# Kernel optimization log

Measured on AMD Instinct MI355X. Metric: run time of the kernel, lower is better.

## Reference

```python
import jax, jax.numpy as jnp
import numpy as np

N_NODES = 20000
N_EDGES = 640000
NUM_COUNTS = 64
NUM_FEATS = 128


def setup_inputs() -> dict:
    key = jax.random.key(0)
    k1, k2, k3, k4, k5 = jax.random.split(key, 5)
    cnt = jax.random.uniform(k1, (N_EDGES, NUM_COUNTS), dtype=jnp.float32)
    embedding = jax.random.normal(k2, (N_NODES, NUM_FEATS), dtype=jnp.float32)
    importance = jax.random.normal(k3, (NUM_COUNTS, NUM_FEATS), dtype=jnp.float32)
    src = jax.random.randint(k4, (N_EDGES,), 0, N_NODES, dtype=jnp.int32)
    # ensure every node has >=1 incoming edge so the normalization divide is well-defined
    dst = jax.random.permutation(k5, jnp.arange(N_EDGES, dtype=jnp.int32) % N_NODES)
    return {"cnt": cnt, "embedding": embedding, "importance": importance, "src": src, "dst": dst}


def reference(cnt, embedding, importance, src, dst):
    # weight = softmax over the num_counts axis (dim=0)
    weight = jax.nn.softmax(importance, axis=0)            # [C, F]
    edge_score = cnt @ weight                               # [E, F] dense GEMM
    msgs = embedding[src] * edge_score                      # [E, F] u_mul_e
    new_embedding = jax.ops.segment_sum(msgs, dst, num_segments=N_NODES)      # [N, F]
    node_score = jax.ops.segment_sum(edge_score, dst, num_segments=N_NODES)   # [N, F]
    return new_embedding / node_score
```

## Files before the change

### kernel.cpp

```cpp
#include <hip/hip_runtime.h>
#include <hip/hip_bf16.h>
#include <stdint.h>

#define NN 20000
#define NE 640000
#define NC 64
#define NF 128
#define CAP 32
#define NPW 5
#define WPB 4
#define NSTEP (2 * NPW)

typedef __attribute__((ext_vector_type(8))) short short8;
typedef __attribute__((ext_vector_type(8))) __bf16 bf16x8;
typedef __attribute__((ext_vector_type(2))) __bf16 bf16x2;
typedef __attribute__((ext_vector_type(4))) float floatx4;
typedef __attribute__((ext_vector_type(4))) unsigned int uintx4;

static __device__ __forceinline__ unsigned short f2bf(float f) {
  union { float f; unsigned int i; } v; v.f = f;
  unsigned int x = v.i;
  x += 0x7fffu + ((x >> 16) & 1u);
  return (unsigned short)(x >> 16);
}

static __device__ __forceinline__ unsigned int pk2(float a, float b) {
#if __has_builtin(__builtin_amdgcn_cvt_pk_bf16_f32)
  bf16x2 r = __builtin_amdgcn_cvt_pk_bf16_f32(a, b);
  return __builtin_bit_cast(unsigned int, r);
#else
  return (unsigned int)f2bf(a) | ((unsigned int)f2bf(b) << 16);
#endif
}

static __device__ __forceinline__ short8 cvt8(floatx4 lo, floatx4 hi) {
  uintx4 u;
  u.x = pk2(lo[0], lo[1]); u.y = pk2(lo[2], lo[3]);
  u.z = pk2(hi[0], hi[1]); u.w = pk2(hi[2], hi[3]);
  return __builtin_bit_cast(short8, u);
}

static __device__ __forceinline__ float frcp(float x) {
#if __has_builtin(__builtin_amdgcn_rcpf)
  return __builtin_amdgcn_rcpf(x);
#else
  return 1.0f / x;
#endif
}

#define GLOAD_LDS(gp, lp)                                                      \
  __builtin_amdgcn_global_load_lds(                                           \
      (const __attribute__((address_space(1))) void*)(gp),                     \
      (__attribute__((address_space(3))) void*)(lp), 16, 0, 0)

__global__ __launch_bounds__(256) void pre_kernel(
    const float* __restrict__ imp, unsigned short* __restrict__ wpack,
    int* __restrict__ counts, int ncounts) {
  __shared__ float w_s[NC][NF];
  const int tid = threadIdx.x;
  for (int i = blockIdx.x * 256 + tid; i < ncounts; i += gridDim.x * 256)
    counts[i] = 0;

  if (blockIdx.x != 0) return;
  if (tid < NF) {
    float v[NC];
    float mx = -1e30f;
#pragma unroll
    for (int c = 0; c < NC; ++c) { v[c] = imp[c * NF + tid]; mx = fmaxf(mx, v[c]); }
    float s = 0.f;
#pragma unroll
    for (int c = 0; c < NC; ++c) { v[c] = __expf(v[c] - mx); s += v[c]; }
    float inv = 1.0f / s;
#pragma unroll
    for (int c = 0; c < NC; ++c) w_s[c][tid] = v[c] * inv;
  }
  __syncthreads();
#pragma unroll
  for (int idx = 0; idx < NC * NF; idx += 256) {
    int i2 = idx + tid;
    int j  = i2 & 7;
    int l  = (i2 >> 3) & 63;
    int ks = (i2 >> 9) & 1;
    int nt = i2 >> 10;
    int k  = ks * 32 + (l >> 4) * 8 + j;
    int f  = 8 * (l & 15) + nt;
    wpack[i2] = f2bf(w_s[k][f]);
  }
}

__global__ __launch_bounds__(256) void bin_kernel(
    const int* __restrict__ dst, int* __restrict__ counts,
    int* __restrict__ elist, int cstride) {
  int e = blockIdx.x * 256 + threadIdx.x;
  if (e < NE) {
    int n = dst[e];
    int slot = atomicAdd(&counts[(size_t)n * cstride], 1);
    if (slot < CAP) elist[n * CAP + slot] = e;
  }
}

__global__ __launch_bounds__(256) void node_kernel(
    const float* __restrict__ cnt,
    const float* __restrict__ emb,
    const int* __restrict__ srcp,
    const int* __restrict__ elist,
    const unsigned short* __restrict__ wpack,
    float* __restrict__ out)
{
  __shared__ float cnt_s[WPB][2][16 * NC];

  const int tid = threadIdx.x;
  const int wid = tid >> 6;
  const int lane = tid & 63;
  const int m = lane & 15;
  const int q = lane >> 4;
  const int base = (blockIdx.x * WPB + wid) * NPW;

  short8 wf[8][2];
#pragma unroll
  for (int nt = 0; nt < 8; ++nt)
#pragma unroll
    for (int ks = 0; ks < 2; ++ks)
      wf[nt][ks] = *(const short8*)(wpack + ((nt * 2 + ks) * 64 + lane) * 8);

  int e_cur = elist[(size_t)base * CAP + (lane & 31)];
  int s_cur = srcp[e_cur];
  int pe = 0, ps = 0;

#pragma unroll
  for (int j = 0; j < 4; ++j) {
    int rl = 4 * j + q;
    int eid = __shfl(e_cur, rl);
    int cs = m ^ (rl & 7);
    GLOAD_LDS(cnt + (size_t)eid * NC + cs * 4, &cnt_s[wid][0][j * 256]);
  }

  float ea[8], sa[8];

#pragma unroll
  for (int s = 0; s < NSTEP; ++s) {
    const int h = s & 1;
    const int node = base + (s >> 1);
    const int cbuf = s & 1;
    const bool more = (s + 1 < NSTEP);

    if (h == 0) {
#pragma unroll
      for (int t = 0; t < 8; ++t) { ea[t] = 0.f; sa[t] = 0.f; }
      if (s + 2 < NSTEP) pe = elist[(size_t)(node + 1) * CAP + (lane & 31)];
    } else if (more) {
      ps = srcp[pe];
    }

    if (more) {
#pragma unroll
      for (int j = 0; j < 4; ++j) {
        int rl = 4 * j + q;
        int eid = __shfl(h ? pe : e_cur, (h ? 0 : 16) + rl);
        int cs = m ^ (rl & 7);
        GLOAD_LDS(cnt + (size_t)eid * NC + cs * 4,
                  &cnt_s[wid][cbuf ^ 1][j * 256]);
      }
      asm volatile("s_waitcnt vmcnt(4)" ::: "memory");
    } else {
      asm volatile("s_waitcnt vmcnt(0)" ::: "memory");
    }

    const float* cb = cnt_s[wid][cbuf];
    const int sw = m & 7;
    const int rb = m * NC;
    floatx4 c0 = *(const floatx4*)&cb[rb + ((2 * q)     ^ sw) * 4];
    floatx4 c1 = *(const floatx4*)&cb[rb + ((2 * q + 1) ^ sw) * 4];
    floatx4 c2 = *(const floatx4*)&cb[rb + ((8 + 2 * q) ^ sw) * 4];
    floatx4 c3 = *(const floatx4*)&cb[rb + ((9 + 2 * q) ^ sw) * 4];
    short8 a0 = cvt8(c0, c1);
    short8 a1 = cvt8(c2, c3);

    floatx4 acc[8];
#pragma unroll
    for (int nt = 0; nt < 8; ++nt) {
#pragma unroll
      for (int r = 0; r < 4; ++r) acc[nt][r] = 0.f;
      acc[nt] = __builtin_amdgcn_mfma_f32_16x16x32_bf16(
          __builtin_bit_cast(bf16x8, a0), __builtin_bit_cast(bf16x8, wf[nt][0]),
          acc[nt], 0, 0, 0);
      acc[nt] = __builtin_amdgcn_mfma_f32_16x16x32_bf16(
          __builtin_bit_cast(bf16x8, a1), __builtin_bit_cast(bf16x8, wf[nt][1]),
          acc[nt], 0, 0, 0);
    }

#pragma unroll
    for (int nt = 0; nt < 8; ++nt)
#pragma unroll
      for (int r = 0; r < 4; ++r) sa[nt] += acc[nt][r];

#pragma unroll
    for (int r = 0; r < 4; ++r) {
      int sv = __shfl(s_cur, h * 16 + 4 * q + r);
      const float* er = emb + (size_t)sv * NF + m * 8;
      floatx4 ev0 = *(const floatx4*)er;
      floatx4 ev1 = *(const floatx4*)(er + 4);
#pragma unroll
      for (int nt = 0; nt < 4; ++nt)
        ea[nt] = fmaf(acc[nt][r], ev0[nt], ea[nt]);
#pragma unroll
      for (int nt = 4; nt < 8; ++nt)
        ea[nt] = fmaf(acc[nt][r], ev1[nt - 4], ea[nt]);
    }

    if (h == 1) {
#pragma unroll
      for (int t = 0; t < 8; ++t) {
        ea[t] += __shfl_xor(ea[t], 16, 64);
        ea[t] += __shfl_xor(ea[t], 32, 64);
        sa[t] += __shfl_xor(sa[t], 16, 64);
        sa[t] += __shfl_xor(sa[t], 32, 64);
      }
      if (lane < 16) {
        floatx4 o0, o1;
#pragma unroll
        for (int p = 0; p < 4; ++p) {
          o0[p] = ea[p] * frcp(sa[p]);
          o1[p] = ea[p + 4] * frcp(sa[p + 4]);
        }
        float* op = out + (size_t)node * NF + m * 8;
        *(floatx4*)op = o0;
        *(floatx4*)(op + 4) = o1;
      }
      if (more) { e_cur = pe; s_cur = ps; }
    }
  }
}

extern "C" void kernel_launch(void* const* d_in, const int* in_sizes, int n_in,
                              void* d_out, int out_size, void* d_ws, size_t ws_size,
                              hipStream_t stream) {
  const float* cnt = (const float*)d_in[0];
  const float* emb = (const float*)d_in[1];
  const float* imp = (const float*)d_in[2];
  const int* src = (const int*)d_in[3];
  const int* dst = (const int*)d_in[4];
  float* out = (float*)d_out;

  char* ws = (char*)d_ws;
  unsigned short* wpack = (unsigned short*)(ws);

  const size_t need_padded = 16384 + (size_t)NN * 32 + (size_t)NN * CAP * 4;
  int cstride;
  int* counts;
  int* elist;
  if (ws_size >= need_padded) {
    cstride = 8;
    counts = (int*)(ws + 16384);
    elist  = (int*)(ws + 16384 + (size_t)NN * 32);
  } else {
    cstride = 1;
    counts = (int*)(ws + 16384);
    elist  = (int*)(ws + 98304);
  }

  const int ncounts = NN * cstride;
  pre_kernel<<<(ncounts + 255) / 256, 256, 0, stream>>>(imp, wpack, counts, ncounts);
  bin_kernel<<<(NE + 255) / 256, 256, 0, stream>>>(dst, counts, elist, cstride);
  node_kernel<<<NN / (WPB * NPW), 256, 0, stream>>>(cnt, emb, src, elist, wpack, out);
}
```

Measured before the change: 309.8 us.

## Pre-convert cnt to bf16 during binning and stage weights in LDS

Binning is fused with a pass that converts the whole fp32 cnt matrix to a bf16 copy in workspace. The node kernel then gathers half-width rows into LDS and reads the packed softmax weights from shared memory instead of holding them in registers. This is meant to cut gather bytes and register pressure in the node kernel. In exchange it adds a full extra read of cnt plus a bf16 write, so total memory traffic goes up. The new path needs a large workspace and falls back to the old fp32 kernel when that is unavailable.

After: 347.3 us. 12.1% more time.

```diff
diff --git a/kernel.cpp b/kernel.cpp
--- a/kernel.cpp
+++ b/kernel.cpp
@@ -88,6 +88,28 @@
   }
 }
 
+__global__ __launch_bounds__(256) void bin_conv_kernel(
+    const float* __restrict__ cnt, const int* __restrict__ dst,
+    int* __restrict__ counts, int* __restrict__ elist,
+    unsigned short* __restrict__ cntbf) {
+  int e = blockIdx.x * 256 + threadIdx.x;
+  if (e >= NE) return;
+  int n = dst[e];
+  int slot = atomicAdd(&counts[(size_t)n * 8], 1);
+  if (slot < CAP) elist[n * CAP + slot] = e;
+
+  const floatx4* s4 = (const floatx4*)(cnt + (size_t)e * NC);
+  uintx4* d4 = (uintx4*)(cntbf + (size_t)e * NC);
+#pragma unroll
+  for (int k = 0; k < 8; ++k) {
+    floatx4 f0 = s4[2 * k], f1 = s4[2 * k + 1];
+    uintx4 u;
+    u.x = pk2(f0[0], f0[1]); u.y = pk2(f0[2], f0[3]);
+    u.z = pk2(f1[0], f1[1]); u.w = pk2(f1[2], f1[3]);
+    d4[k] = u;
+  }
+}
+
 __global__ __launch_bounds__(256) void bin_kernel(
     const int* __restrict__ dst, int* __restrict__ counts,
     int* __restrict__ elist, int cstride) {
@@ -100,14 +122,15 @@
 }
 
 __global__ __launch_bounds__(256) void node_kernel(
-    const float* __restrict__ cnt,
+    const unsigned short* __restrict__ cntbf,
     const float* __restrict__ emb,
     const int* __restrict__ srcp,
     const int* __restrict__ elist,
     const unsigned short* __restrict__ wpack,
     float* __restrict__ out)
 {
-  __shared__ float cnt_s[WPB][2][16 * NC];
+  __shared__ short cnt_s[WPB][2][16 * NC];
+  __shared__ short wpack_s[NC * NF];
 
   const int tid = threadIdx.x;
   const int wid = tid >> 6;
@@ -116,6 +139,133 @@
   const int q = lane >> 4;
   const int base = (blockIdx.x * WPB + wid) * NPW;
 
+#pragma unroll
+  for (int k = 0; k < 4; ++k) {
+    int idx = (tid * 4 + k) * 8;
+    *(short8*)&wpack_s[idx] = *(const short8*)&wpack[idx];
+  }
+  __syncthreads();
+
+  int e_cur = elist[(size_t)base * CAP + (lane & 31)];
+  int s_cur = srcp[e_cur];
+  int pe = 0, ps = 0;
+
+  const int rr = lane >> 3;
+  const int pp = lane & 7;
+
+#pragma unroll
+  for (int j = 0; j < 2; ++j) {
+    int row = j * 8 + rr;
+    int eid = __shfl(e_cur, row);
+    int c = pp ^ (row & 7);
+    GLOAD_LDS(cntbf + (size_t)eid * NC + c * 8, &cnt_s[wid][0][j * 512]);
+  }
+
+  float ea[8], sa[8];
+
+#pragma unroll
+  for (int s = 0; s < NSTEP; ++s) {
+    const int h = s & 1;
+    const int node = base + (s >> 1);
+    const int cbuf = s & 1;
+    const bool more = (s + 1 < NSTEP);
+
+    if (h == 0) {
+#pragma unroll
+      for (int t = 0; t < 8; ++t) { ea[t] = 0.f; sa[t] = 0.f; }
+      if (s + 2 < NSTEP) pe = elist[(size_t)(node + 1) * CAP + (lane & 31)];
+    } else if (more) {
+      ps = srcp[pe];
+    }
+
+    if (more) {
+#pragma unroll
+      for (int j = 0; j < 2; ++j) {
+        int row = j * 8 + rr;
+        int eid = __shfl(h ? pe : e_cur, (h ? 0 : 16) + row);
+        int c = pp ^ (row & 7);
+        GLOAD_LDS(cntbf + (size_t)eid * NC + c * 8,
+                  &cnt_s[wid][cbuf ^ 1][j * 512]);
+      }
+      asm volatile("s_waitcnt vmcnt(2)" ::: "memory");
+    } else {
+      asm volatile("s_waitcnt vmcnt(0)" ::: "memory");
+    }
+
+    const short* cb = cnt_s[wid][cbuf];
+    short8 a0 = *(const short8*)&cb[m * NC + ((q       ^ (m & 7)) * 8)];
+    short8 a1 = *(const short8*)&cb[m * NC + (((4 + q) ^ (m & 7)) * 8)];
+
+    floatx4 acc[8];
+#pragma unroll
+    for (int nt = 0; nt < 8; ++nt) {
+#pragma unroll
+      for (int r = 0; r < 4; ++r) acc[nt][r] = 0.f;
+      short8 w0 = *(const short8*)&wpack_s[((nt * 2 + 0) * 64 + lane) * 8];
+      short8 w1 = *(const short8*)&wpack_s[((nt * 2 + 1) * 64 + lane) * 8];
+      acc[nt] = __builtin_amdgcn_mfma_f32_16x16x32_bf16(
+          __builtin_bit_cast(bf16x8, a0), __builtin_bit_cast(bf16x8, w0),
+          acc[nt], 0, 0, 0);
+      acc[nt] = __builtin_amdgcn_mfma_f32_16x16x32_bf16(
+          __builtin_bit_cast(bf16x8, a1), __builtin_bit_cast(bf16x8, w1),
+          acc[nt], 0, 0, 0);
+    }
+
+#pragma unroll
+    for (int nt = 0; nt < 8; ++nt)
+#pragma unroll
+      for (int r = 0; r < 4; ++r) sa[nt] += acc[nt][r];
+
+#pragma unroll
+    for (int r = 0; r < 4; ++r) {
+      int sv = __shfl(s_cur, h * 16 + 4 * q + r);
+      const float* er = emb + (size_t)sv * NF + m * 8;
+      floatx4 ev0 = *(const floatx4*)er;
+      floatx4 ev1 = *(const floatx4*)(er + 4);
+#pragma unroll
+      for (int nt = 0; nt < 4; ++nt)
+        ea[nt] = fmaf(acc[nt][r], ev0[nt], ea[nt]);
+#pragma unroll
+      for (int nt = 4; nt < 8; ++nt)
+        ea[nt] = fmaf(acc[nt][r], ev1[nt - 4], ea[nt]);
+    }
+
+    if (h == 1) {
+#pragma unroll
+      for (int t = 0; t < 8; ++t) {
+        ea[t] += __shfl_xor(ea[t], 16, 64);
+        ea[t] += __shfl_xor(ea[t], 32, 64);
+        sa[t] += __shfl_xor(sa[t], 16, 64);
+        sa[t] += __shfl_xor(sa[t], 32, 64);
+      }
+      if (lane < 16) {
+        floatx4 o0, o1;
+#pragma unroll
+        for (int p = 0; p < 4; ++p) {
+          o0[p] = ea[p] * frcp(sa[p]);
+          o1[p] = ea[p + 4] * frcp(sa[p + 4]);
+        }
+        float* op = out + (size_t)node * NF + m * 8;
+        *(floatx4*)op = o0;
+        *(floatx4*)(op + 4) = o1;
+      }
+      if (more) { e_cur = pe; s_cur = ps; }
+    }
+  }
+}
+
+__global__ __launch_bounds__(256) void node_kernel_f32(
+    const float* __restrict__ cnt, const float* __restrict__ emb,
+    const int* __restrict__ srcp, const int* __restrict__ elist,
+    const unsigned short* __restrict__ wpack, float* __restrict__ out) {
+  __shared__ float cnt_s[WPB][2][16 * NC];
+  const int tid = threadIdx.x;
+  const int wid = tid >> 6;
+  const int lane = tid & 63;
+  const int m = lane & 15;
+  const int q = lane >> 4;
+  const int base = (blockIdx.x * WPB + wid) * NPW;
+
   short8 wf[8][2];
 #pragma unroll
   for (int nt = 0; nt < 8; ++nt)
@@ -136,14 +286,12 @@
   }
 
   float ea[8], sa[8];
-
 #pragma unroll
   for (int s = 0; s < NSTEP; ++s) {
     const int h = s & 1;
     const int node = base + (s >> 1);
     const int cbuf = s & 1;
     const bool more = (s + 1 < NSTEP);
-
     if (h == 0) {
 #pragma unroll
       for (int t = 0; t < 8; ++t) { ea[t] = 0.f; sa[t] = 0.f; }
@@ -151,31 +299,27 @@
     } else if (more) {
       ps = srcp[pe];
     }
-
     if (more) {
 #pragma unroll
       for (int j = 0; j < 4; ++j) {
         int rl = 4 * j + q;
         int eid = __shfl(h ? pe : e_cur, (h ? 0 : 16) + rl);
         int cs = m ^ (rl & 7);
-        GLOAD_LDS(cnt + (size_t)eid * NC + cs * 4,
-                  &cnt_s[wid][cbuf ^ 1][j * 256]);
+        GLOAD_LDS(cnt + (size_t)eid * NC + cs * 4, &cnt_s[wid][cbuf ^ 1][j * 256]);
       }
       asm volatile("s_waitcnt vmcnt(4)" ::: "memory");
     } else {
       asm volatile("s_waitcnt vmcnt(0)" ::: "memory");
     }
-
     const float* cb = cnt_s[wid][cbuf];
     const int sw = m & 7;
     const int rb = m * NC;
-    floatx4 c0 = *(const floatx4*)&cb[rb + ((2 * q)     ^ sw) * 4];
+    floatx4 c0 = *(const floatx4*)&cb[rb + ((2 * q) ^ sw) * 4];
     floatx4 c1 = *(const floatx4*)&cb[rb + ((2 * q + 1) ^ sw) * 4];
     floatx4 c2 = *(const floatx4*)&cb[rb + ((8 + 2 * q) ^ sw) * 4];
     floatx4 c3 = *(const floatx4*)&cb[rb + ((9 + 2 * q) ^ sw) * 4];
     short8 a0 = cvt8(c0, c1);
     short8 a1 = cvt8(c2, c3);
-
     floatx4 acc[8];
 #pragma unroll
     for (int nt = 0; nt < 8; ++nt) {
@@ -188,12 +332,10 @@
           __builtin_bit_cast(bf16x8, a1), __builtin_bit_cast(bf16x8, wf[nt][1]),
           acc[nt], 0, 0, 0);
     }
-
 #pragma unroll
     for (int nt = 0; nt < 8; ++nt)
 #pragma unroll
       for (int r = 0; r < 4; ++r) sa[nt] += acc[nt][r];
-
 #pragma unroll
     for (int r = 0; r < 4; ++r) {
       int sv = __shfl(s_cur, h * 16 + 4 * q + r);
@@ -201,13 +343,10 @@
       floatx4 ev0 = *(const floatx4*)er;
       floatx4 ev1 = *(const floatx4*)(er + 4);
 #pragma unroll
-      for (int nt = 0; nt < 4; ++nt)
-        ea[nt] = fmaf(acc[nt][r], ev0[nt], ea[nt]);
-#pragma unroll
-      for (int nt = 4; nt < 8; ++nt)
-        ea[nt] = fmaf(acc[nt][r], ev1[nt - 4], ea[nt]);
-    }
-
+      for (int nt = 0; nt < 4; ++nt) ea[nt] = fmaf(acc[nt][r], ev0[nt], ea[nt]);
+#pragma unroll
+      for (int nt = 4; nt < 8; ++nt) ea[nt] = fmaf(acc[nt][r], ev1[nt - 4], ea[nt]);
+    }
     if (h == 1) {
 #pragma unroll
       for (int t = 0; t < 8; ++t) {
@@ -244,23 +383,25 @@
 
   char* ws = (char*)d_ws;
   unsigned short* wpack = (unsigned short*)(ws);
-
-  const size_t need_padded = 16384 + (size_t)NN * 32 + (size_t)NN * CAP * 4;
-  int cstride;
-  int* counts;
-  int* elist;
-  if (ws_size >= need_padded) {
-    cstride = 8;
-    counts = (int*)(ws + 16384);
-    elist  = (int*)(ws + 16384 + (size_t)NN * 32);
+  int* counts = (int*)(ws + 16384);
+  int* elist  = (int*)(ws + 16384 + (size_t)NN * 32);
+
+  const size_t CNTBF_OFF = 4u << 20;
+  const size_t need_bf16 = CNTBF_OFF + (size_t)NE * NC * 2;
+  unsigned short* cntbf = (unsigned short*)(ws + CNTBF_OFF);
+
+  if (ws_size >= need_bf16) {
+    const int ncounts = NN * 8;
+    pre_kernel<<<(ncounts + 255) / 256, 256, 0, stream>>>(imp, wpack, counts, ncounts);
+    bin_conv_kernel<<<(NE + 255) / 256, 256, 0, stream>>>(cnt, dst, counts, elist, cntbf);
+    node_kernel<<<NN / (WPB * NPW), 256, 0, stream>>>(cntbf, emb, src, elist, wpack, out);
   } else {
-    cstride = 1;
-    counts = (int*)(ws + 16384);
-    elist  = (int*)(ws + 98304);
-  }
-
-  const int ncounts = NN * cstride;
-  pre_kernel<<<(ncounts + 255) / 256, 256, 0, stream>>>(imp, wpack, counts, ncounts);
-  bin_kernel<<<(NE + 255) / 256, 256, 0, stream>>>(dst, counts, elist, cstride);
-  node_kernel<<<NN / (WPB * NPW), 256, 0, stream>>>(cnt, emb, src, elist, wpack, out);
-}
+    const size_t need_padded = 16384 + (size_t)NN * 32 + (size_t)NN * CAP * 4;
+    int cstride = (ws_size >= need_padded) ? 8 : 1;
+    if (cstride == 1) { counts = (int*)(ws + 16384); elist = (int*)(ws + 98304); }
+    const int ncounts = NN * cstride;
+    pre_kernel<<<(ncounts + 255) / 256, 256, 0, stream>>>(imp, wpack, counts, ncounts);
+    bin_kernel<<<(NE + 255) / 256, 256, 0, stream>>>(dst, counts, elist, cstride);
+    node_kernel_f32<<<NN / (WPB * NPW), 256, 0, stream>>>(cnt, emb, src, elist, wpack, out);
+  }
+}
```
